# Kernel tuning notes

Measured on AMD Instinct MI355X. Metric: run time of the kernel, lower is better.

## Reference

```python
import jax, jax.numpy as jnp
import numpy as np

NUM_CLASSES = 21
IOU_THR = 0.5
SCORE_THR = 0.04


def _conv(x, w, b, stride):
    # NCHW / OIHW, SAME padding
    y = jax.lax.conv_general_dilated(
        x, w, (stride, stride), 'SAME',
        dimension_numbers=('NCHW', 'OIHW', 'NCHW'))
    return y + b[None, :, None, None]


def _pairwise_iou(boxes):
    # original module which feeds locs straight into ops.nms.
    x1, y1, x2, y2 = boxes[:, 0], boxes[:, 1], boxes[:, 2], boxes[:, 3]
    area = (x2 - x1) * (y2 - y1)
    lt_x = jnp.maximum(x1[:, None], x1[None, :])
    lt_y = jnp.maximum(y1[:, None], y1[None, :])
    rb_x = jnp.minimum(x2[:, None], x2[None, :])
    rb_y = jnp.minimum(y2[:, None], y2[None, :])
    inter = jnp.clip(rb_x - lt_x, 0.0) * jnp.clip(rb_y - lt_y, 0.0)
    union = area[:, None] + area[None, :] - inter
    return inter / (union + 1e-9)


def _nms_keep(boxes, scores, valid):
    # Greedy NMS over score-sorted candidates; padded/masked, jit-friendly.
    order = jnp.argsort(-scores)
    b = boxes[order]            # [N,4]
    v = valid[order]            # [N]
    iou = _pairwise_iou(b)      # [N,N]
    n = boxes.shape[0]

    def body(i, keep):
        suppressed = jnp.any(keep & (iou[i] > IOU_THR))
        return keep.at[i].set(v[i] & jnp.logical_not(suppressed))

    keep = jax.lax.fori_loop(0, n, body, jnp.zeros((n,), bool))
    return order, keep


def _ssd_forward(x, bb_w1, bb_b1, bb_w2, bb_b2, bb_w3, bb_b3,
                 ex_w, ex_b, reg_w, reg_b, cls_w, cls_b):
    # backbone: three stride-2 conv+relu blocks
    h = jax.nn.relu(_conv(x, bb_w1, bb_b1, 2))
    h = jax.nn.relu(_conv(h, bb_w2, bb_b2, 2))
    h = jax.nn.relu(_conv(h, bb_w3, bb_b3, 2))
    # extras: one stride-2 conv+relu
    h = jax.nn.relu(_conv(h, ex_w, ex_b, 2))
    # heads
    locs = _conv(h, reg_w, reg_b, 1)    # [B, 4, H, W]
    confs = _conv(h, cls_w, cls_b, 1)   # [B, C, H, W]
    B = locs.shape[0]
    locs = jnp.transpose(locs, (0, 2, 3, 1)).reshape(B, -1, 4)        # [B, N, 4]
    confs = jnp.transpose(confs, (0, 2, 3, 1)).reshape(B, -1, NUM_CLASSES)  # [B, N, C]

    # PostProcessor: softmax -> max -> threshold mask -> NMS, vectorized over batch
    probs = jax.nn.softmax(confs, axis=-1)
    scores = jnp.max(probs, axis=-1)      # [B, N]
    labels = jnp.argmax(probs, axis=-1)   # [B, N]
    valid = scores > SCORE_THR

    order, keep = jax.vmap(_nms_keep)(locs, scores, valid)  # [B,N], [B,N] bool

    # The original's buggy inner loop leaves only the LAST image's results.
    i = B - 1
    o, k = order[i], keep[i]
    b_s = locs[i][o]
    s_s = scores[i][o]
    l_s = labels[i][o]
    c_s = confs[i][o]
    out_boxes = jnp.where(k[:, None], b_s, -1.0)
    out_labels = jnp.where(k, l_s, 0).astype(jnp.int64)
    out_scores = jnp.where(k, s_s, -1.0)
    out_confs = jnp.where(k[:, None], c_s, -1.0)
    return out_boxes, out_labels, out_scores, out_confs


def setup_inputs() -> dict:
    key = jax.random.key(0)
    ks = jax.random.split(key, 8)

    def w(k, shape):
        fan_in = shape[1] * shape[2] * shape[3]
        return jax.random.normal(k, shape, jnp.float32) / np.sqrt(fan_in)

    x = jax.random.normal(ks[0], (8, 3, 512, 512), jnp.float32)
    return {
        'x': x,
        'bb_w1': w(ks[1], (64, 3, 3, 3)),   'bb_b1': jnp.zeros((64,), jnp.float32),
        'bb_w2': w(ks[2], (128, 64, 3, 3)), 'bb_b2': jnp.zeros((128,), jnp.float32),
        'bb_w3': w(ks[3], (256, 128, 3, 3)),'bb_b3': jnp.zeros((256,), jnp.float32),
        'ex_w':  w(ks[4], (256, 256, 3, 3)),'ex_b':  jnp.zeros((256,), jnp.float32),
        'reg_w': w(ks[5], (4, 256, 3, 3)),  'reg_b': jnp.zeros((4,), jnp.float32),
        'cls_w': w(ks[6], (NUM_CLASSES, 256, 3, 3)), 'cls_b': jnp.zeros((NUM_CLASSES,), jnp.float32),
    }


def reference(x, bb_w1, bb_b1, bb_w2, bb_b2, bb_w3, bb_b3,
              ex_w, ex_b, reg_w, reg_b, cls_w, cls_b):
    return _ssd_forward(x, bb_w1, bb_b1, bb_w2, bb_b2, bb_w3, bb_b3,
                        ex_w, ex_b, reg_w, reg_b, cls_w, cls_b)
```

## Files before the change

### kernel.cpp

```cpp
#include <hip/hip_runtime.h>
#include <cstdint>
#include <cstddef>


__global__ __launch_bounds__(256) void k_repack_all(
    const float* __restrict__ w2, const float* __restrict__ w3,
    const float* __restrict__ w4, const float* __restrict__ regw,
    const float* __restrict__ clsw, float* __restrict__ wr2,
    float* __restrict__ wr3, float* __restrict__ wr4, float* __restrict__ wh) {
  int idx = blockIdx.x * 256 + threadIdx.x;
  if (idx < 73728) {
    int co = idx % 128, r = idx / 128, ci = r / 9, tap = r % 9;
    wr2[idx] = w2[(co * 64 + ci) * 9 + tap];
  } else if (idx < 73728 + 294912) {
    int i = idx - 73728;
    int co = i % 256, r = i / 256, ci = r / 9, tap = r % 9;
    wr3[i] = w3[(co * 128 + ci) * 9 + tap];
  } else if (idx < 73728 + 294912 + 589824) {
    int i = idx - (73728 + 294912);
    int co = i % 256, r = i / 256, ci = r / 9, tap = r % 9;
    wr4[i] = w4[(co * 256 + ci) * 9 + tap];
  } else if (idx < 73728 + 294912 + 589824 + 57600) {
    int i = idx - (73728 + 294912 + 589824);
    int ci = i & 255, r = i >> 8, tap = r / 25, o = r % 25;
    wh[i] = (o < 4) ? regw[(o * 256 + ci) * 9 + tap]
                    : clsw[((o - 4) * 256 + ci) * 9 + tap];
  }
}

__global__ __launch_bounds__(256) void k_conv1(const float* __restrict__ x,
                                               const float* __restrict__ w,
                                               const float* __restrict__ b,
                                               float* __restrict__ out) {
  __shared__ float in_t[3][33][33];
  const int tx = threadIdx.x, ty = threadIdx.y;
  const int tid = ty * 16 + tx;
  const int ox0 = blockIdx.x * 16, oy0 = blockIdx.y * 16;
  const int co0 = blockIdx.z * 8;
  for (int idx = tid; idx < 3 * 33 * 33; idx += 256) {
    int ci = idx / 1089, rem = idx % 1089;
    int r = rem / 33, c = rem % 33;
    int iy = oy0 * 2 + r, ix = ox0 * 2 + c;
    float v = 0.f;
    if (iy < 512 && ix < 512) v = x[(size_t)ci * 262144 + iy * 512 + ix];
    in_t[ci][r][c] = v;
  }
  __syncthreads();
  float rin[27];
#pragma unroll
  for (int ci = 0; ci < 3; ++ci)
#pragma unroll
    for (int kh = 0; kh < 3; ++kh)
#pragma unroll
      for (int kw = 0; kw < 3; ++kw)
        rin[ci * 9 + kh * 3 + kw] = in_t[ci][2 * ty + kh][2 * tx + kw];
  const int oy = oy0 + ty, ox = ox0 + tx;
  for (int co = co0; co < co0 + 8; ++co) {
    float a = 0.f;
#pragma unroll
    for (int k = 0; k < 27; ++k) a = fmaf(w[co * 27 + k], rin[k], a);
    out[(size_t)co * 65536 + oy * 256 + ox] = fmaxf(a + b[co], 0.f);
  }
}

template <int CIN, int COUT, int HIN, int WIN, int SH, int SW, int COPT,
          int CIT, int KSPLIT, int ROWW, int NW>
__global__ __launch_bounds__(NW * 64, 4) void conv_s2(
    const float* __restrict__ in, const float* __restrict__ wr,
    const float* __restrict__ bias, float* __restrict__ out) {
  constexpr int HOUT = HIN / 2, WOUT = WIN / 2;
  constexpr int IH = SH * 2 + 1, IW = SW * 2 + 1;
  constexpr int EVW = SW + 1;
  constexpr int COT = NW * COPT;
  constexpr int NPAIR = CIT * IH * EVW;
  constexpr int NTHR = NW * 64;
  constexpr int NLD = (NPAIR + NTHR - 1) / NTHR;
  constexpr int NC4 = COPT / 4;
  constexpr int CO4 = COT / 4;
  constexpr int W4  = CIT * 9 * CO4;
  constexpr int NLW = (W4 + NTHR - 1) / NTHR;
  static_assert(SH * SW == 64, "one position per lane");
  static_assert(EVW + SW < ROWW + 1, "pad slot fits");
  static_assert(COPT % 4 == 0, "float4 weight chunks");
  __shared__ float lds[CIT * IH * ROWW];
  __shared__ float4 wlds4[W4];

  const int tid = threadIdx.x;
  const int gu  = __builtin_amdgcn_readfirstlane(tid >> 6);
  const int lp  = tid & 63;
  const int py  = lp / SW, px = lp % SW;

  constexpr int ntx = WOUT / SW;
  const int bx = blockIdx.x % ntx, by = blockIdx.x / ntx;
  const int ox0 = bx * SW, oy0 = by * SH;
  const int co_blk = blockIdx.y * COT;
  const int cobase = co_blk + gu * COPT;
  const int ci_begin = (KSPLIT > 1) ? blockIdx.z * (CIN / KSPLIT) : 0;
  constexpr int NST = (CIN / KSPLIT) / CIT;

  unsigned goff[NLD];
  int      loff[NLD];
  int      mode[NLD];
#pragma unroll
  for (int j = 0; j < NLD; ++j) {
    int idx = tid + j * NTHR;
    bool act = (idx < NPAIR);
    int ci = idx / (IH * EVW), rem = idx % (IH * EVW);
    int r = rem / EVW, c2 = rem % EVW;
    int iy = oy0 * 2 + r, ix = ox0 * 2 + 2 * c2;
    loff[j] = act ? (ci * IH + r) * ROWW + c2 : -1;
    goff[j] = (unsigned)((ci_begin + ci) * HIN * WIN + iy * WIN + ix);
    int m = 0;
    if (act && iy < HIN) {
      if ((2 * c2 + 1 < IW) && (ix + 1 < WIN)) m = 1;
      else if (ix < WIN) m = 2;
    }
    mode[j] = m;
  }

  unsigned wgoff[NLW];
  bool     wok[NLW];
#pragma unroll
  for (int j = 0; j < NLW; ++j) {
    int widx = tid + j * NTHR;
    wok[j] = (widx < W4);
    int row = widx / CO4, cw4 = widx % CO4;
    wgoff[j] = (unsigned)((ci_begin * 9 + row) * COUT + co_blk + cw4 * 4);
  }

  float2 pre[NLD];
#pragma unroll
  for (int j = 0; j < NLD; ++j) {
    float2 t = make_float2(0.f, 0.f);
    if (mode[j] == 1)      t = *(const float2*)(in + goff[j]);
    else if (mode[j] == 2) t.x = in[goff[j]];
    pre[j] = t;
  }
  float4 wpre[NLW];
#pragma unroll
  for (int j = 0; j < NLW; ++j)
    if (wok[j]) wpre[j] = *(const float4*)(wr + wgoff[j]);

  float acc[COPT] = {};

  constexpr unsigned IADV = (unsigned)(CIT * HIN * WIN);
  constexpr unsigned WADV = (unsigned)(CIT * 9 * COUT);
  unsigned iadv = IADV, wadv = WADV;
  for (int st = 0; st < NST; ++st, iadv += IADV, wadv += WADV) {
    if (st) __syncthreads();
#pragma unroll
    for (int j = 0; j < NLD; ++j) {
      if (loff[j] >= 0) {
        lds[loff[j]] = pre[j].x;
        lds[loff[j] + EVW] = pre[j].y;
      }
    }
#pragma unroll
    for (int j = 0; j < NLW; ++j)
      if (wok[j]) wlds4[tid + j * NTHR] = wpre[j];
    __syncthreads();
    if (st + 1 < NST) {
#pragma unroll
      for (int j = 0; j < NLD; ++j) {
        float2 t = make_float2(0.f, 0.f);
        if (mode[j] == 1)      t = *(const float2*)(in + goff[j] + iadv);
        else if (mode[j] == 2) t.x = in[goff[j] + iadv];
        pre[j] = t;
      }
#pragma unroll
      for (int j = 0; j < NLW; ++j)
        if (wok[j]) wpre[j] = *(const float4*)(wr + wgoff[j] + wadv);
    }
#pragma unroll 2
    for (int ci = 0; ci < CIT; ++ci) {
      const int b0 = (ci * IH + 2 * py) * ROWW + px;
      float in9[9];
      in9[0] = lds[b0];
      in9[1] = lds[b0 + EVW];
      in9[2] = lds[b0 + 1];
      in9[3] = lds[b0 + ROWW];
      in9[4] = lds[b0 + ROWW + EVW];
      in9[5] = lds[b0 + ROWW + 1];
      in9[6] = lds[b0 + 2 * ROWW];
      in9[7] = lds[b0 + 2 * ROWW + EVW];
      in9[8] = lds[b0 + 2 * ROWW + 1];
      const int wb = ci * 9 * CO4 + gu * NC4;
#pragma unroll
      for (int t = 0; t < 9; ++t) {
#pragma unroll
        for (int q = 0; q < NC4; ++q) {
          float4 wv = wlds4[wb + t * CO4 + q];
          acc[q * 4 + 0] = fmaf(in9[t], wv.x, acc[q * 4 + 0]);
          acc[q * 4 + 1] = fmaf(in9[t], wv.y, acc[q * 4 + 1]);
          acc[q * 4 + 2] = fmaf(in9[t], wv.z, acc[q * 4 + 2]);
          acc[q * 4 + 3] = fmaf(in9[t], wv.w, acc[q * 4 + 3]);
        }
      }
    }
  }

  const int oy = oy0 + py, ox = ox0 + px;
#pragma unroll
  for (int c = 0; c < COPT; ++c) {
    int co = cobase + c;
    if constexpr (KSPLIT > 1) {
      out[((size_t)blockIdx.z * COUT + co) * (HOUT * WOUT) + oy * WOUT + ox] =
          acc[c];
    } else {
      out[(size_t)co * (HOUT * WOUT) + oy * WOUT + ox] =
          fmaxf(acc[c] + bias[co], 0.f);
    }
  }
}

__global__ __launch_bounds__(256) void k_combine(const float* __restrict__ part,
                                                 const float* __restrict__ b,
                                                 float* __restrict__ h4t) {
  int co = blockIdx.x;
  float bb = b[co];
  for (int k2 = 0; k2 < 4; ++k2) {
    int pos = threadIdx.x + k2 * 256;
    float v = part[(size_t)(0 * 256 + co) * 1024 + pos] +
              part[(size_t)(1 * 256 + co) * 1024 + pos] +
              part[(size_t)(2 * 256 + co) * 1024 + pos] +
              part[(size_t)(3 * 256 + co) * 1024 + pos];
    h4t[(size_t)pos * 256 + co] = fmaxf(v + bb, 0.f);
  }
}

__global__ __launch_bounds__(256) void k_head(const float* __restrict__ h4t,
                                              const float* __restrict__ wh,
                                              const float* __restrict__ regb,
                                              const float* __restrict__ clsb,
                                              float* __restrict__ locs,
                                              float* __restrict__ confs,
                                              float* __restrict__ scores,
                                              float* __restrict__ labelsF) {
  const int pos = blockIdx.x;
  const int py = pos >> 5, px = pos & 31;
  const int t = threadIdx.x;
  float part[25] = {};
#pragma unroll
  for (int kh = 0; kh < 3; ++kh) {
    int iy = py + kh - 1;
    if (iy < 0 || iy > 31) continue;
#pragma unroll
    for (int kw = 0; kw < 3; ++kw) {
      int ix = px + kw - 1;
      if (ix < 0 || ix > 31) continue;
      int tap = kh * 3 + kw;
      float v = h4t[(size_t)(iy * 32 + ix) * 256 + t];
      const float* wp = wh + (size_t)tap * 25 * 256 + t;
#pragma unroll
      for (int o = 0; o < 25; ++o)
        part[o] = fmaf(v, wp[(size_t)o * 256], part[o]);
    }
  }
#pragma unroll
  for (int o = 0; o < 25; ++o) {
#pragma unroll
    for (int d = 1; d < 64; d <<= 1) part[o] += __shfl_xor(part[o], d);
  }
  __shared__ float red[4][25];
  __shared__ float yv[25];
  const int wv = t >> 6, ln = t & 63;
  if (ln == 0) {
#pragma unroll
    for (int o = 0; o < 25; ++o) red[wv][o] = part[o];
  }
  __syncthreads();
  if (t < 25) {
    float y = red[0][t] + red[1][t] + red[2][t] + red[3][t];
    y += (t < 4) ? regb[t] : clsb[t - 4];
    if (t < 4) locs[(size_t)pos * 4 + t] = y;
    else       confs[(size_t)pos * 21 + (t - 4)] = y;
    yv[t] = y;
  }
  __syncthreads();
  if (t == 0) {
    float m = yv[4];
    int lab = 0;
    for (int j = 1; j < 21; ++j)
      if (yv[4 + j] > m) { m = yv[4 + j]; lab = j; }
    float s = 0.f;
    for (int j = 0; j < 21; ++j) s += expf(yv[4 + j] - m);
    scores[pos] = 1.f / s;
    labelsF[pos] = (float)lab;
  }
}

__global__ __launch_bounds__(512) void k_sort(const float* __restrict__ scores,
                                              const float* __restrict__ locs,
                                              int* __restrict__ order,
                                              float* __restrict__ ssc,
                                              float* __restrict__ bsrt,
                                              unsigned long long* __restrict__ vbits) {
  __shared__ float sk[1024];
  __shared__ int   si[1024];
  const int t = threadIdx.x;
  sk[t] = scores[t];           si[t] = t;
  sk[t + 512] = scores[t + 512]; si[t + 512] = t + 512;
  for (int k = 2; k <= 1024; k <<= 1) {
    for (int j = k >> 1; j > 0; j >>= 1) {
      __syncthreads();
      int i1 = ((t / j) * (2 * j)) + (t % j);
      int i2 = i1 + j;
      bool up = (i1 & k) == 0;
      float sa = sk[i1], sb = sk[i2];
      int ia = si[i1], ib = si[i2];
      bool b_before_a = (sb > sa) || (sb == sa && ib < ia);
      bool a_before_b = (sa > sb) || (sa == sb && ia < ib);
      bool sw = up ? b_before_a : a_before_b;
      if (sw) { sk[i1] = sb; sk[i2] = sa; si[i1] = ib; si[i2] = ia; }
    }
  }
  __syncthreads();
  for (int i = t; i < 1024; i += 512) {
    int oi = si[i];
    order[i] = oi;
    ssc[i] = sk[i];
    ((float4*)bsrt)[i] = ((const float4*)locs)[oi];
  }
  if (t < 16) {
    unsigned long long w = 0;
    for (int b2 = 0; b2 < 64; ++b2)
      if (sk[t * 64 + b2] > 0.04f) w |= (1ull << b2);
    vbits[t] = w;
  }
}

__global__ __launch_bounds__(256) void k_mask(const float* __restrict__ bsrt,
                                              unsigned long long* __restrict__ mask) {
  __shared__ float4 sb[1024];
  const int t = threadIdx.x;
  for (int idx = t; idx < 1024; idx += 256)
    sb[idx] = ((const float4*)bsrt)[idx];
  __syncthreads();
  const int i = blockIdx.x * 16 + (t & 15);
  const int w = t >> 4;
  float4 bi = sb[i];
  float ai = (bi.z - bi.x) * (bi.w - bi.y);
  unsigned long long bits = 0;
  for (int jj = 0; jj < 64; ++jj) {
    float4 bj = sb[w * 64 + jj];
    float aj = (bj.z - bj.x) * (bj.w - bj.y);
    float ltx = fmaxf(bi.x, bj.x), lty = fmaxf(bi.y, bj.y);
    float rbx = fminf(bi.z, bj.z), rby = fminf(bi.w, bj.w);
    float inter = fmaxf(rbx - ltx, 0.f) * fmaxf(rby - lty, 0.f);
    float uni = ai + aj - inter;
    float iou = inter / (uni + 1e-9f);
    if (iou > 0.5f) bits |= (1ull << jj);
  }
  mask[(size_t)i * 16 + w] = bits;
}

__global__ __launch_bounds__(1024) void k_nms_gather(
    const unsigned long long* __restrict__ mask,
    const unsigned long long* __restrict__ vbits,
    const int* __restrict__ order, const float* __restrict__ ssc,
    const float* __restrict__ locs, const float* __restrict__ confs,
    const float* __restrict__ labelsF, float* __restrict__ out) {
  __shared__ unsigned long long KEEP[16], DEAD[16];
  __shared__ int ncert;
  const int i = threadIdx.x;
  const int w = i >> 6, l = i & 63;

  unsigned long long R[16];
#pragma unroll
  for (int k = 0; k < 16; ++k) {
    unsigned long long m = 0;
    if (k < w) m = mask[(size_t)i * 16 + k];
    else if (k == w && l) m = mask[(size_t)i * 16 + k] & ((1ull << l) - 1ull);
    R[k] = m;
  }
  const bool valid = (vbits[w] >> l) & 1ull;

  if (i < 16) { KEEP[i] = 0ull; DEAD[i] = 0ull; }
  if (i == 0) ncert = 0;
  __syncthreads();

  int status = 0;
  for (;;) {
    unsigned long long s = 0, p = 0;
    if (status == 0) {
#pragma unroll
      for (int k = 0; k < 16; ++k) {
        unsigned long long K_ = KEEP[k], D_ = DEAD[k];
        s |= R[k] & K_;
        p |= R[k] & ~D_;
      }
    }
    __syncthreads();
    bool newKeep = false, newDead = false;
    if (status == 0) {
      if (!valid)      { status = 2; newDead = true; }
      else if (s)      { status = 2; newDead = true; }
      else if (!p)     { status = 1; newKeep = true; }
    }
    unsigned long long bk = __ballot(newKeep);
    unsigned long long bd = __ballot(newDead);
    if (l == 0) {
      if (bk) KEEP[w] |= bk;
      if (bd) DEAD[w] |= bd;
      int n = __popcll(bk) + __popcll(bd);
      if (n) atomicAdd(&ncert, n);
    }
    __syncthreads();
    if (ncert >= 1024) break;
  }

  const bool kp = (status == 1);
  const int oi = order[i];
  float4 bx = kp ? ((const float4*)locs)[oi]
                 : make_float4(-1.f, -1.f, -1.f, -1.f);
  ((float4*)out)[i] = bx;
  out[4096 + i] = kp ? labelsF[oi] : 0.f;
  out[5120 + i] = kp ? ssc[i] : -1.f;
  float* oc = out + 6144 + (size_t)i * 21;
  const float* cc = confs + (size_t)oi * 21;
#pragma unroll
  for (int c = 0; c < 21; ++c) oc[c] = kp ? cc[c] : -1.f;
}

extern "C" void kernel_launch(void* const* d_in, const int* in_sizes, int n_in,
                              void* d_out, int out_size, void* d_ws, size_t ws_size,
                              hipStream_t stream) {
  const float* x    = (const float*)d_in[0] + (size_t)7 * 3 * 512 * 512;
  const float* w1   = (const float*)d_in[1];
  const float* b1   = (const float*)d_in[2];
  const float* w2   = (const float*)d_in[3];
  const float* b2   = (const float*)d_in[4];
  const float* w3   = (const float*)d_in[5];
  const float* b3   = (const float*)d_in[6];
  const float* w4   = (const float*)d_in[7];
  const float* b4   = (const float*)d_in[8];
  const float* regw = (const float*)d_in[9];
  const float* regb = (const float*)d_in[10];
  const float* clsw = (const float*)d_in[11];
  const float* clsb = (const float*)d_in[12];
  float* out = (float*)d_out;
  char* ws = (char*)d_ws;

  float* h1    = (float*)(ws + 0);
  float* part4 = (float*)(ws + 0);
  float* h4t   = (float*)(ws + 9437184);
  float* h2    = (float*)(ws + 16777216);
  float* h3    = (float*)(ws + 25165824);
  float* wr2   = (float*)(ws + 29360128);
  float* wr3   = (float*)(ws + 29655040);
  float* wr4   = (float*)(ws + 30834688);
  float* wh    = (float*)(ws + 33193984);
  float* locs  = (float*)(ws + 33424384);
  float* confs = (float*)(ws + 33440768);
  float* scores  = (float*)(ws + 33526784);
  float* labelsF = (float*)(ws + 33530880);
  int*   order   = (int*)  (ws + 33534976);
  float* ssc     = (float*)(ws + 33539072);
  float* bsrt    = (float*)(ws + 33543168);
  unsigned long long* mask  = (unsigned long long*)(ws + 33559552);
  unsigned long long* vbits = (unsigned long long*)(ws + 33690624);

  k_repack_all<<<3969, 256, 0, stream>>>(w2, w3, w4, regw, clsw,
                                         wr2, wr3, wr4, wh);

  k_conv1<<<dim3(16, 16, 8), dim3(16, 16), 0, stream>>>(x, w1, b1, h1);

  conv_s2<64, 128, 256, 256, 4, 16, 8, 16, 1, 36, 4>
      <<<dim3(256, 4, 1), 256, 0, stream>>>(h1, wr2, b2, h2);
  conv_s2<128, 256, 128, 128, 8, 8, 4, 16, 1, 20, 4>
      <<<dim3(64, 16, 1), 256, 0, stream>>>(h2, wr3, b3, h3);
  conv_s2<256, 256, 64, 64, 8, 8, 4, 16, 4, 20, 4>
      <<<dim3(16, 16, 4), 256, 0, stream>>>(h3, wr4, (const float*)nullptr, part4);
  k_combine<<<256, 256, 0, stream>>>(part4, b4, h4t);

  k_head<<<1024, 256, 0, stream>>>(h4t, wh, regb, clsb, locs, confs, scores, labelsF);

  k_sort<<<1, 512, 0, stream>>>(scores, locs, order, ssc, bsrt, vbits);
  k_mask<<<64, 256, 0, stream>>>(bsrt, mask);
  k_nms_gather<<<1, 1024, 0, stream>>>(mask, vbits, order, ssc, locs, confs,
                                       labelsF, out);
}
```

Baseline: 408.3 us.

## Stream conv weights straight into double-buffered LDS via global_load_lds

For the two deeper stride-2 convs, weight tiles are now fetched with async global-to-LDS loads into a double-buffered shared array. This replaces the old register prefetch followed by an LDS store. The first conv instead skips weight staging and reads wave-uniform weights directly from global memory inside the FMA loop. The goal is to cut register pressure and the extra LDS store pass, and to overlap weight fetch with compute. The cost is double the weight LDS footprint and a reliance on correct wait/barrier ordering for the async LDS writes.

```diff
diff --git a/kernel.cpp b/kernel.cpp
--- a/kernel.cpp
+++ b/kernel.cpp
@@ -64,7 +64,7 @@
 }
 
 template <int CIN, int COUT, int HIN, int WIN, int SH, int SW, int COPT,
-          int CIT, int KSPLIT, int ROWW, int NW>
+          int CIT, int KSPLIT, int ROWW, int NW, int WLDS>
 __global__ __launch_bounds__(NW * 64, 4) void conv_s2(
     const float* __restrict__ in, const float* __restrict__ wr,
     const float* __restrict__ bias, float* __restrict__ out) {
@@ -78,12 +78,12 @@
   constexpr int NC4 = COPT / 4;
   constexpr int CO4 = COT / 4;
   constexpr int W4  = CIT * 9 * CO4;
-  constexpr int NLW = (W4 + NTHR - 1) / NTHR;
   static_assert(SH * SW == 64, "one position per lane");
   static_assert(EVW + SW < ROWW + 1, "pad slot fits");
   static_assert(COPT % 4 == 0, "float4 weight chunks");
+  static_assert(!WLDS || (W4 % 64 == 0), "whole lane-rounds");
   __shared__ float lds[CIT * IH * ROWW];
-  __shared__ float4 wlds4[W4];
+  __shared__ float4 wlds4[WLDS ? 2 * W4 : 1];
 
   const int tid = threadIdx.x;
   const int gu  = __builtin_amdgcn_readfirstlane(tid >> 6);
@@ -97,6 +97,22 @@
   const int cobase = co_blk + gu * COPT;
   const int ci_begin = (KSPLIT > 1) ? blockIdx.z * (CIN / KSPLIT) : 0;
   constexpr int NST = (CIN / KSPLIT) / CIT;
+
+  auto wload = [&](int cibN, int bsel) {
+#pragma unroll
+    for (int r = 0; r < W4 / 64; ++r) {
+      if ((r & (NW - 1)) == gu) {
+        int f4 = r * 64 + lp;
+        int row = f4 / CO4, c4 = f4 % CO4;
+        const float* g =
+            wr + (size_t)(cibN * 9 + row) * COUT + co_blk + c4 * 4;
+        __builtin_amdgcn_global_load_lds(
+            (const __attribute__((address_space(1))) void*)g,
+            (__attribute__((address_space(3))) void*)&wlds4[bsel * W4 + r * 64],
+            16, 0, 0);
+      }
+    }
+  };
 
   unsigned goff[NLD];
   int      loff[NLD];
@@ -118,16 +134,7 @@
     mode[j] = m;
   }
 
-  unsigned wgoff[NLW];
-  bool     wok[NLW];
-#pragma unroll
-  for (int j = 0; j < NLW; ++j) {
-    int widx = tid + j * NTHR;
-    wok[j] = (widx < W4);
-    int row = widx / CO4, cw4 = widx % CO4;
-    wgoff[j] = (unsigned)((ci_begin * 9 + row) * COUT + co_blk + cw4 * 4);
-  }
-
+  if constexpr (WLDS) wload(ci_begin, 0);
   float2 pre[NLD];
 #pragma unroll
   for (int j = 0; j < NLD; ++j) {
@@ -136,17 +143,13 @@
     else if (mode[j] == 2) t.x = in[goff[j]];
     pre[j] = t;
   }
-  float4 wpre[NLW];
-#pragma unroll
-  for (int j = 0; j < NLW; ++j)
-    if (wok[j]) wpre[j] = *(const float4*)(wr + wgoff[j]);
 
   float acc[COPT] = {};
 
   constexpr unsigned IADV = (unsigned)(CIT * HIN * WIN);
-  constexpr unsigned WADV = (unsigned)(CIT * 9 * COUT);
-  unsigned iadv = IADV, wadv = WADV;
-  for (int st = 0; st < NST; ++st, iadv += IADV, wadv += WADV) {
+  unsigned iadv = IADV;
+  for (int st = 0; st < NST; ++st, iadv += IADV) {
+    const int cib = ci_begin + st * CIT;
     if (st) __syncthreads();
 #pragma unroll
     for (int j = 0; j < NLD; ++j) {
@@ -155,11 +158,9 @@
         lds[loff[j] + EVW] = pre[j].y;
       }
     }
-#pragma unroll
-    for (int j = 0; j < NLW; ++j)
-      if (wok[j]) wlds4[tid + j * NTHR] = wpre[j];
     __syncthreads();
     if (st + 1 < NST) {
+      if constexpr (WLDS) wload(cib + CIT, (st + 1) & 1);
 #pragma unroll
       for (int j = 0; j < NLD; ++j) {
         float2 t = make_float2(0.f, 0.f);
@@ -167,9 +168,6 @@
         else if (mode[j] == 2) t.x = in[goff[j] + iadv];
         pre[j] = t;
       }
-#pragma unroll
-      for (int j = 0; j < NLW; ++j)
-        if (wok[j]) wpre[j] = *(const float4*)(wr + wgoff[j] + wadv);
     }
 #pragma unroll 2
     for (int ci = 0; ci < CIT; ++ci) {
@@ -184,17 +182,27 @@
       in9[6] = lds[b0 + 2 * ROWW];
       in9[7] = lds[b0 + 2 * ROWW + EVW];
       in9[8] = lds[b0 + 2 * ROWW + 1];
-      const int wb = ci * 9 * CO4 + gu * NC4;
-#pragma unroll
-      for (int t = 0; t < 9; ++t) {
-#pragma unroll
-        for (int q = 0; q < NC4; ++q) {
-          float4 wv = wlds4[wb + t * CO4 + q];
-          acc[q * 4 + 0] = fmaf(in9[t], wv.x, acc[q * 4 + 0]);
-          acc[q * 4 + 1] = fmaf(in9[t], wv.y, acc[q * 4 + 1]);
-          acc[q * 4 + 2] = fmaf(in9[t], wv.z, acc[q * 4 + 2]);
-          acc[q * 4 + 3] = fmaf(in9[t], wv.w, acc[q * 4 + 3]);
+      if constexpr (WLDS) {
+        const float4* wb = &wlds4[(st & 1) * W4];
+        const int wrow = ci * 9 * CO4 + gu * NC4;
+#pragma unroll
+        for (int t = 0; t < 9; ++t) {
+#pragma unroll
+          for (int q = 0; q < NC4; ++q) {
+            float4 wv = wb[wrow + t * CO4 + q];
+            acc[q * 4 + 0] = fmaf(in9[t], wv.x, acc[q * 4 + 0]);
+            acc[q * 4 + 1] = fmaf(in9[t], wv.y, acc[q * 4 + 1]);
+            acc[q * 4 + 2] = fmaf(in9[t], wv.z, acc[q * 4 + 2]);
+            acc[q * 4 + 3] = fmaf(in9[t], wv.w, acc[q * 4 + 3]);
+          }
         }
+      } else {
+        const float* wp = wr + (size_t)(cib + ci) * 9 * COUT + cobase;
+#pragma unroll
+        for (int t = 0; t < 9; ++t)
+#pragma unroll
+          for (int c = 0; c < COPT; ++c)
+            acc[c] = fmaf(in9[t], wp[t * COUT + c], acc[c]);
       }
     }
   }
@@ -465,11 +473,11 @@
 
   k_conv1<<<dim3(16, 16, 8), dim3(16, 16), 0, stream>>>(x, w1, b1, h1);
 
-  conv_s2<64, 128, 256, 256, 4, 16, 8, 16, 1, 36, 4>
+  conv_s2<64, 128, 256, 256, 4, 16, 8, 16, 1, 36, 4, 0>
       <<<dim3(256, 4, 1), 256, 0, stream>>>(h1, wr2, b2, h2);
-  conv_s2<128, 256, 128, 128, 8, 8, 4, 16, 1, 20, 4>
+  conv_s2<128, 256, 128, 128, 8, 8, 4, 16, 1, 20, 4, 1>
       <<<dim3(64, 16, 1), 256, 0, stream>>>(h2, wr3, b3, h3);
-  conv_s2<256, 256, 64, 64, 8, 8, 4, 16, 4, 20, 4>
+  conv_s2<256, 256, 64, 64, 8, 8, 4, 16, 4, 20, 4, 1>
       <<<dim3(16, 16, 4), 256, 0, stream>>>(h3, wr4, (const float*)nullptr, part4);
   k_combine<<<256, 256, 0, stream>>>(part4, b4, h4t);
 
```

Result: faster. 357.3 us (-12.5%).
